# Kernel tuning notes

Hardware: AMD Instinct MI355X
Metric: run time of the kernel (lower is better)

## Reference

```python
import jax, jax.numpy as jnp
import numpy as np

B, L, D, H = 4, 2048, 2048, 16
HD = D // H
EPS = 1e-6


def _rope_tables(l, hd, base=10000.0):
    inv = 1.0 / (base ** (np.arange(0, hd, 2, dtype=np.float32) / hd))  # [hd/2]
    t = np.arange(l, dtype=np.float32)
    ang = np.outer(t, inv)  # [l, hd/2]
    return jnp.asarray(np.cos(ang)), jnp.asarray(np.sin(ang))


def setup_inputs() -> dict:
    key = jax.random.key(0)
    ks = jax.random.split(key, 8)
    cos, sin = _rope_tables(L, HD)
    s = 1.0 / np.sqrt(D)
    return {
        "x": jax.random.normal(ks[0], (B, L, D), jnp.float32),
        "freqs_cos": cos,
        "freqs_sin": sin,
        "Wqk": jax.random.normal(ks[1], (D, 2 * D), jnp.float32) * s,
        "Wv": jax.random.normal(ks[2], (D, D), jnp.float32) * s,
        "bv": jax.random.normal(ks[3], (D,), jnp.float32) * 0.02,
        "Wp": jax.random.normal(ks[4], (D, D), jnp.float32) * s,
        "bp": jax.random.normal(ks[5], (D,), jnp.float32) * 0.02,
        "qn_w": jnp.ones((HD,), jnp.float32),
        "kn_w": jnp.ones((HD,), jnp.float32),
    }


def _rmsnorm(x, w, eps=EPS):
    ms = jnp.mean(jnp.square(x), axis=-1, keepdims=True)
    return x * jax.lax.rsqrt(ms + eps) * w


def _rope(x, cos, sin):
    # x: [b,h,l,hd]; cos/sin: [l,hd/2]; interleaved (complex) rotation
    x1 = x[..., 0::2]
    x2 = x[..., 1::2]
    c = cos[None, None, :, :]
    s = sin[None, None, :, :]
    out = jnp.stack([x1 * c - x2 * s, x1 * s + x2 * c], axis=-1)
    return out.reshape(x.shape)


def reference(x, freqs_cos, freqs_sin, Wqk, Wv, bv, Wp, bp, qn_w, kn_w):
    b, l, d = x.shape
    qk = x @ Wqk  # [b,l,2d]
    q, k = jnp.split(qk, 2, axis=-1)
    v = x @ Wv + bv
    # [b,l,d] -> [b,h,l,hd]
    to_heads = lambda t: t.reshape(b, l, H, HD).transpose(0, 2, 1, 3)
    q, k, v = to_heads(q), to_heads(k), to_heads(v)
    q = _rmsnorm(q, qn_w)
    k = _rmsnorm(k, kn_w)
    q = _rope(q, freqs_cos, freqs_sin)
    k = _rope(k, freqs_cos, freqs_sin)
    scale = 1.0 / jnp.sqrt(jnp.asarray(HD, q.dtype))
    scores = jnp.einsum("bhqd,bhkd->bhqk", q, k) * scale
    causal = jnp.tril(jnp.ones((l, l), bool))
    scores = jnp.where(causal[None, None], scores, jnp.asarray(-1e30, scores.dtype))
    attn = jax.nn.softmax(scores, axis=-1)
    y = jnp.einsum("bhqk,bhkd->bhqd", attn, v)
    y = y.transpose(0, 2, 1, 3).reshape(b, l, d)
    return y @ Wp + bp
```

## Files before the change

kernel.cpp:

```cpp
#include <hip/hip_runtime.h>
#include <hip/hip_bf16.h>
#include <math.h>

#define B_  4
#define L_  2048
#define D_  2048
#define H_  16
#define HD_ 128
#define BH_ (B_*H_)
#define BL_ (B_*L_)

typedef __attribute__((ext_vector_type(4))) float  f32x4;
typedef __attribute__((ext_vector_type(8))) __bf16 bf16x8;

static __device__ __forceinline__ float bf2f(unsigned short u) {
    union { unsigned int i; float f; } v; v.i = ((unsigned int)u) << 16; return v.f;
}
static __device__ __forceinline__ unsigned short f2bf(float f) {
    union { float f; unsigned int i; } v; v.f = f;
    unsigned int x = v.i;
    return (unsigned short)((x + 0x7fffu + ((x >> 16) & 1u)) >> 16);
}

static __device__ __forceinline__ void gload16(const unsigned short* g, unsigned short* l) {
    __builtin_amdgcn_global_load_lds(
        (const __attribute__((address_space(1))) unsigned int*)(const void*)g,
        (__attribute__((address_space(3))) unsigned int*)(void*)l, 16, 0, 0);
}

__global__ __launch_bounds__(256) void k_f32_to_bf16(const float* __restrict__ s,
                                                     unsigned short* __restrict__ d, int n8) {
    int i = blockIdx.x * 256 + threadIdx.x;
    if (i >= n8) return;
    const float* p = s + (size_t)i * 8;
    float4 a = *(const float4*)p;
    float4 b = *(const float4*)(p + 4);
    union { bf16x8 v; unsigned short u[8]; } o;
    o.u[0]=f2bf(a.x); o.u[1]=f2bf(a.y); o.u[2]=f2bf(a.z); o.u[3]=f2bf(a.w);
    o.u[4]=f2bf(b.x); o.u[5]=f2bf(b.y); o.u[6]=f2bf(b.z); o.u[7]=f2bf(b.w);
    *(bf16x8*)(d + (size_t)i * 8) = o.v;
}

__global__ __launch_bounds__(256) void k_transpose_f2b(const float* __restrict__ src,
                                                       unsigned short* __restrict__ dst,
                                                       int R, int C, int dstStride) {
    __shared__ float tile[32][33];
    int tx = threadIdx.x & 31, ty = threadIdx.x >> 5;
    int c0 = blockIdx.x * 32, r0 = blockIdx.y * 32;
    #pragma unroll
    for (int i = 0; i < 32; i += 8)
        tile[ty + i][tx] = src[(size_t)(r0 + ty + i) * C + c0 + tx];
    __syncthreads();
    #pragma unroll
    for (int i = 0; i < 32; i += 8)
        dst[(size_t)(c0 + ty + i) * dstStride + r0 + tx] = f2bf(tile[tx][ty + i]);
}

__global__ __launch_bounds__(256) void k_transpose_v(const unsigned short* __restrict__ vb,
                                                     unsigned short* __restrict__ vT) {
    __shared__ unsigned short tile[32][33];
    int bh = blockIdx.z;
    int hd0 = blockIdx.x * 32, l0 = blockIdx.y * 32;
    int tx = threadIdx.x & 31, ty = threadIdx.x >> 5;
    const unsigned short* in = vb + (size_t)bh * L_ * HD_;
    unsigned short* out      = vT + (size_t)bh * L_ * HD_;
    #pragma unroll
    for (int i = 0; i < 32; i += 8)
        tile[ty + i][tx] = in[(size_t)(l0 + ty + i) * HD_ + hd0 + tx];
    __syncthreads();
    #pragma unroll
    for (int i = 0; i < 32; i += 8)
        out[(size_t)(hd0 + ty + i) * L_ + l0 + tx] = tile[tx][ty + i];
}

template<int MG, int NG>
static __device__ __forceinline__ void mfma_quad(const bf16x8 (&afr)[4][2],
                                                 const bf16x8 (&bfr)[2][2],
                                                 f32x4 (&acc)[8][4]) {
    #pragma unroll
    for (int mi = 0; mi < 4; ++mi)
        #pragma unroll
        for (int ni = 0; ni < 2; ++ni) {
            acc[MG*4+mi][NG*2+ni] = __builtin_amdgcn_mfma_f32_16x16x32_bf16(
                afr[mi][0], bfr[ni][0], acc[MG*4+mi][NG*2+ni], 0, 0, 0);
            acc[MG*4+mi][NG*2+ni] = __builtin_amdgcn_mfma_f32_16x16x32_bf16(
                afr[mi][1], bfr[ni][1], acc[MG*4+mi][NG*2+ni], 0, 0, 0);
        }
}

static __device__ __forceinline__ void ds_load_a(const unsigned short* u, int wm,
                                                 int l15, int l4, bf16x8 (&afr)[4][2]) {
    int sw = l15 & 7;
    #pragma unroll
    for (int mi = 0; mi < 4; ++mi) {
        int ro = (wm*64 + mi*16 + l15) * 64;
        afr[mi][0] = *(const bf16x8*)(u + ro + ((l4 ^ sw) << 3));
        afr[mi][1] = *(const bf16x8*)(u + ro + (((4 + l4) ^ sw) << 3));
    }
}

static __device__ __forceinline__ void ds_load_b(const unsigned short* u, int wn,
                                                 int l15, int l4, bf16x8 (&bfr)[2][2]) {
    int sw = l15 & 7;
    #pragma unroll
    for (int ni = 0; ni < 2; ++ni) {
        int ro = (wn*32 + ni*16 + l15) * 64;
        bfr[ni][0] = *(const bf16x8*)(u + ro + ((l4 ^ sw) << 3));
        bfr[ni][1] = *(const bf16x8*)(u + ro + (((4 + l4) ^ sw) << 3));
    }
}

#define STAGE_A_(c_, mg_, t_) do {                                                        \
    gload16(gA + (size_t)(((mg_)*64      ) * 2048) + (t_)*64, &Lds[c_][0][mg_][w*512]);   \
    gload16(gA + (size_t)(((mg_)*64 + 128) * 2048) + (t_)*64, &Lds[c_][0][mg_][4096 + w*512]); \
} while (0)
#define STAGE_B_(c_, ng_, t_) do {                                                        \
    gload16(gB + (size_t)(((ng_)*32 + ((w>>2)    )*64) * 2048) + (t_)*64, &Lds[c_][1][ng_][w*512]); \
    gload16(gB + (size_t)(((ng_)*32 + ((w>>2) + 2)*64) * 2048) + (t_)*64, &Lds[c_][1][ng_][4096 + w*512]); \
} while (0)
#define SB_() __builtin_amdgcn_sched_barrier(0)

template<int MODE>
__global__ __launch_bounds__(512, 2) void k_gemm(const unsigned short* __restrict__ A,
                                                 const unsigned short* __restrict__ Bt,
                                                 int M, int N, int K,
                                                 const float* __restrict__ bias,
                                                 unsigned short* __restrict__ qout,
                                                 unsigned short* __restrict__ kout,
                                                 unsigned short* __restrict__ vout,
                                                 float* __restrict__ fout) {
    (void)K;
    __shared__ __align__(16) unsigned short Lds[2][2][2][8192];
    const int tid = threadIdx.x;
    const int lane = tid & 63, w = tid >> 6;
    const int wm = w >> 2, wn = w & 3;
    const int l15 = lane & 15, l4 = lane >> 4;
    const int lsw = (lane & 7) ^ ((lane >> 3) & 7);

    int nwgx = gridDim.x;
    int bid = blockIdx.y * nwgx + blockIdx.x;
    int cpx = (nwgx * gridDim.y) >> 3;
    int sb = (bid & 7) * cpx + (bid >> 3);
    int n0 = (sb % nwgx) * 256, m0 = (sb / nwgx) * 256;

    const unsigned short* gA = A  + (size_t)(m0 + w*8 + (lane >> 3)) * 2048 + lsw*8;
    const unsigned short* gB = Bt + (size_t)(n0 + (w&3)*8 + (lane >> 3)) * 2048 + lsw*8;

    f32x4 acc[8][4] = {};
    bf16x8 afr[4][2], bf0[2][2], bf1[2][2];
    const int nt = 2048 / 64;

    STAGE_A_(0, 0, 0); STAGE_B_(0, 0, 0); STAGE_B_(0, 1, 0); STAGE_A_(0, 1, 0);
    STAGE_A_(1, 0, 1); STAGE_B_(1, 0, 1); STAGE_B_(1, 1, 1);
    asm volatile("s_waitcnt vmcnt(6)" ::: "memory");
    __builtin_amdgcn_s_barrier();

    for (int t = 0; t < nt; ++t) {
        const int c = t & 1, cn = c ^ 1;
        const bool h1 = (t + 1 < nt), h2 = (t + 2 < nt);

        ds_load_a(&Lds[c][0][0][0], wm, l15, l4, afr);
        ds_load_b(&Lds[c][1][0][0], wn, l15, l4, bf0);
        SB_();
        ds_load_b(&Lds[c][1][1][0], wn, l15, l4, bf1);
        SB_();
        if (h1) STAGE_A_(cn, 1, t + 1);
        __builtin_amdgcn_s_barrier();
        asm volatile("s_waitcnt lgkmcnt(4)" ::: "memory");
        SB_();
        __builtin_amdgcn_s_setprio(1);
        mfma_quad<0, 0>(afr, bf0, acc);
        __builtin_amdgcn_s_setprio(0);
        SB_();
        __builtin_amdgcn_s_barrier();

        asm volatile("s_waitcnt lgkmcnt(0)" ::: "memory");
        SB_();
        __builtin_amdgcn_s_setprio(1);
        mfma_quad<0, 1>(afr, bf1, acc);
        __builtin_amdgcn_s_setprio(0);
        SB_();
        ds_load_a(&Lds[c][0][1][0], wm, l15, l4, afr);
        SB_();
        if (h2) STAGE_A_(c, 0, t + 2);
        __builtin_amdgcn_s_barrier();

        if (h2) STAGE_B_(c, 0, t + 2);
        asm volatile("s_waitcnt lgkmcnt(0)" ::: "memory");
        SB_();
        __builtin_amdgcn_s_setprio(1);
        mfma_quad<1, 1>(afr, bf1, acc);
        __builtin_amdgcn_s_setprio(0);
        SB_();
        if (h2) STAGE_B_(c, 1, t + 2);
        __builtin_amdgcn_s_setprio(1);
        mfma_quad<1, 0>(afr, bf0, acc);
        __builtin_amdgcn_s_setprio(0);
        SB_();
        if (h2) asm volatile("s_waitcnt vmcnt(4)" ::: "memory");
        else    asm volatile("s_waitcnt vmcnt(0)" ::: "memory");
        __builtin_amdgcn_s_barrier();
    }

    #pragma unroll
    for (int mi = 0; mi < 8; ++mi) {
        #pragma unroll
        for (int ni = 0; ni < 4; ++ni) {
            int ncol = n0 + wn*64 + ni*16 + l15;
            #pragma unroll
            for (int j = 0; j < 4; ++j) {
                int m = m0 + wm*128 + mi*16 + l4*4 + j;
                float v = acc[mi][ni][j];
                if (MODE == 0) {
                    int b = m >> 11, l = m & 2047;
                    if (ncol < 2048) {
                        int h = ncol >> 7, hd = ncol & 127;
                        qout[((size_t)(b*H_ + h) * L_ + l) * HD_ + hd] = f2bf(v);
                    } else if (ncol < 4096) {
                        int cc = ncol - 2048, h = cc >> 7, hd = cc & 127;
                        kout[((size_t)(b*H_ + h) * L_ + l) * HD_ + hd] = f2bf(v);
                    } else {
                        int cc = ncol - 4096, h = cc >> 7, hd = cc & 127;
                        vout[((size_t)(b*H_ + h) * L_ + l) * HD_ + hd] = f2bf(v + bias[cc]);
                    }
                } else {
                    fout[(size_t)m * N + ncol] = v + bias[ncol];
                }
            }
        }
    }
}

__global__ __launch_bounds__(256) void k_normrope(unsigned short* __restrict__ qb,
                                                  unsigned short* __restrict__ kb,
                                                  const float* __restrict__ cosT,
                                                  const float* __restrict__ sinT,
                                                  const float* __restrict__ qw,
                                                  const float* __restrict__ kw) {
    const float QSCL = 0.08838834764831845f * 1.4426950408889634f;
    int lane = threadIdx.x & 63;
    int row = blockIdx.x * 4 + (threadIdx.x >> 6);
    int isK = row >= BH_ * L_;
    unsigned short* buf = isK ? kb : qb;
    const float* w = isK ? kw : qw;
    int r = isK ? row - BH_ * L_ : row;
    int l = r & (L_ - 1);
    unsigned short* p = buf + (size_t)r * HD_ + lane * 2;
    ushort2 u = *(const ushort2*)p;
    float x1 = bf2f(u.x), x2 = bf2f(u.y);
    float ss = x1*x1 + x2*x2;
    #pragma unroll
    for (int off = 32; off; off >>= 1) ss += __shfl_xor(ss, off);
    float rs = rsqrtf(ss * (1.0f / 128.0f) + 1e-6f);
    rs *= isK ? 1.0f : QSCL;
    float c = cosT[l * 64 + lane], s = sinT[l * 64 + lane];
    float y1 = x1 * rs * w[lane * 2];
    float y2 = x2 * rs * w[lane * 2 + 1];
    ushort2 o;
    o.x = f2bf(y1 * c - y2 * s);
    o.y = f2bf(y1 * s + y2 * c);
    *(ushort2*)p = o;
}

#define PLDT 72

__global__ __launch_bounds__(256) void k_attn(const unsigned short* __restrict__ qbuf,
                                              const unsigned short* __restrict__ kbuf,
                                              const unsigned short* __restrict__ vT,
                                              unsigned short* __restrict__ yb) {
    __shared__ __align__(16) unsigned short Ks[64 * 128];
    __shared__ __align__(16) unsigned short Vs[128 * 64];
    __shared__ __align__(16) unsigned short Ps[4][32 * PLDT];
    int tid = threadIdx.x, lane = tid & 63, w = tid >> 6;
    int l15 = lane & 15, l4 = lane >> 4;
    int qb = 15 - (blockIdx.x >> 6);
    int bh = blockIdx.x & 63;
    const unsigned short* Q  = qbuf + (size_t)bh * L_ * HD_;
    const unsigned short* Kp = kbuf + (size_t)bh * L_ * HD_;
    const unsigned short* Vp = vT   + (size_t)bh * L_ * HD_;
    int qr0 = qb * 128 + w * 32;

    bf16x8 qf[2][4];
    #pragma unroll
    for (int m = 0; m < 2; ++m)
        #pragma unroll
        for (int ks = 0; ks < 4; ++ks)
            qf[m][ks] = *(const bf16x8*)(Q + (size_t)(qr0 + m*16 + l15) * HD_ + ks*32 + l4*8);

    f32x4 accO[2][8] = {};
    f32x4 accW[2] = {};

    bf16x8 vones;
    #pragma unroll
    for (int i = 0; i < 8; ++i) vones[i] = (__bf16)1.0f;

    const float BOUND = 20.0f;
    int nkt = 2 * qb + 2;

    for (int kt = 0; kt < nkt; ++kt) {
        int kbase = kt * 64;
        #pragma unroll
        for (int i = 0; i < 4; ++i) {
            int g = w * 4 + i;
            int kr = g * 4 + (lane >> 4);
            gload16(Kp + (size_t)(kbase + kr) * HD_ + (((lane & 15) ^ (kr & 15)) << 3),
                    Ks + g * 512);
            int vr = g * 8 + (lane >> 3);
            gload16(Vp + (size_t)vr * L_ + kbase + (((lane & 7) ^ (vr & 7)) << 3),
                    Vs + g * 512);
        }
        __syncthreads();

        if (kbase <= qr0 + 31) {
            f32x4 sf[2][4] = {};
            #pragma unroll
            for (int f = 0; f < 4; ++f)
                #pragma unroll
                for (int ks = 0; ks < 4; ++ks) {
                    bf16x8 kf = *(const bf16x8*)(Ks + (f*16 + l15) * 128 +
                                                 ((((ks*4) + l4) ^ l15) << 3));
                    sf[0][f] = __builtin_amdgcn_mfma_f32_16x16x32_bf16(qf[0][ks], kf, sf[0][f], 0, 0, 0);
                    sf[1][f] = __builtin_amdgcn_mfma_f32_16x16x32_bf16(qf[1][ks], kf, sf[1][f], 0, 0, 0);
                }

            unsigned short* ps = Ps[w];
            #pragma unroll
            for (int m = 0; m < 2; ++m) {
                bool needmask = (kbase + 63 > qr0 + m*16);
                #pragma unroll
                for (int f = 0; f < 4; ++f)
                    #pragma unroll
                    for (int j = 0; j < 4; ++j) {
                        float s = sf[m][f][j];
                        if (needmask) {
                            int key  = kbase + f*16 + l15;
                            int qrow = qr0 + m*16 + l4*4 + j;
                            if (key > qrow) s = -1e30f;
                        }
                        float p = exp2f(s - BOUND);
                        *(__bf16*)(ps + (m*16 + l4*4 + j) * PLDT + f*16 + l15) = (__bf16)p;
                    }
            }

            #pragma unroll
            for (int ks = 0; ks < 2; ++ks) {
                bf16x8 pa0 = *(const bf16x8*)(ps + l15 * PLDT + ks*32 + l4*8);
                bf16x8 pa1 = *(const bf16x8*)(ps + (16 + l15) * PLDT + ks*32 + l4*8);
                #pragma unroll
                for (int cf = 0; cf < 8; ++cf) {
                    bf16x8 vf = *(const bf16x8*)(Vs + (cf*16 + l15) * 64 +
                                                 ((((ks*4) + l4) ^ (l15 & 7)) << 3));
                    accO[0][cf] = __builtin_amdgcn_mfma_f32_16x16x32_bf16(pa0, vf, accO[0][cf], 0, 0, 0);
                    accO[1][cf] = __builtin_amdgcn_mfma_f32_16x16x32_bf16(pa1, vf, accO[1][cf], 0, 0, 0);
                }
                accW[0] = __builtin_amdgcn_mfma_f32_16x16x32_bf16(pa0, vones, accW[0], 0, 0, 0);
                accW[1] = __builtin_amdgcn_mfma_f32_16x16x32_bf16(pa1, vones, accW[1], 0, 0, 0);
            }
        }
        __syncthreads();
    }

    int b = bh >> 4, h = bh & 15;
    #pragma unroll
    for (int m = 0; m < 2; ++m)
        #pragma unroll
        for (int cf = 0; cf < 8; ++cf)
            #pragma unroll
            for (int j = 0; j < 4; ++j) {
                int qrow = qr0 + m*16 + l4*4 + j;
                float o = accO[m][cf][j] / accW[m][j];
                yb[((size_t)(b * L_ + qrow)) * D_ + h*128 + cf*16 + l15] = f2bf(o);
            }
}

extern "C" void kernel_launch(void* const* d_in, const int* in_sizes, int n_in,
                              void* d_out, int out_size, void* d_ws, size_t ws_size,
                              hipStream_t stream) {
    const float* x    = (const float*)d_in[0];
    const float* fcos = (const float*)d_in[1];
    const float* fsin = (const float*)d_in[2];
    const float* Wqk  = (const float*)d_in[3];
    const float* Wv   = (const float*)d_in[4];
    const float* bv   = (const float*)d_in[5];
    const float* Wp   = (const float*)d_in[6];
    const float* bp   = (const float*)d_in[7];
    const float* qn_w = (const float*)d_in[8];
    const float* kn_w = (const float*)d_in[9];
    float* out = (float*)d_out;

    char* ws = (char*)d_ws;
    unsigned short* Wt   = (unsigned short*)(ws);
    unsigned short* Wpt  = (unsigned short*)(ws + 25165824);
    unsigned short* xb   = (unsigned short*)(ws + 33554432);
    unsigned short* qbuf = (unsigned short*)(ws + 67108864);
    unsigned short* kbuf = (unsigned short*)(ws + 100663296);
    unsigned short* vbuf = (unsigned short*)(ws + 134217728);
    unsigned short* vTb  = (unsigned short*)(ws + 167772160);
    unsigned short* yb   = xb;

    k_f32_to_bf16<<<8192, 256, 0, stream>>>(x, xb, BL_ * D_ / 8);
    k_transpose_f2b<<<dim3(128, 64), 256, 0, stream>>>(Wqk, Wt, 2048, 4096, 2048);
    k_transpose_f2b<<<dim3(64, 64),  256, 0, stream>>>(Wv,  Wt + (size_t)4096 * 2048, 2048, 2048, 2048);
    k_transpose_f2b<<<dim3(64, 64),  256, 0, stream>>>(Wp,  Wpt, 2048, 2048, 2048);

    k_gemm<0><<<dim3(24, 32), 512, 0, stream>>>(xb, Wt, BL_, 6144, 2048, bv,
                                                qbuf, kbuf, vbuf, nullptr);
    k_normrope<<<2 * BH_ * L_ / 4, 256, 0, stream>>>(qbuf, kbuf, fcos, fsin, qn_w, kn_w);
    k_transpose_v<<<dim3(4, 64, 64), 256, 0, stream>>>(vbuf, vTb);
    k_attn<<<BH_ * (L_ / 128), 256, 0, stream>>>(qbuf, kbuf, vTb, yb);
    k_gemm<1><<<dim3(8, 32), 512, 0, stream>>>(yb, Wpt, BL_, 2048, 2048, bp,
                                               nullptr, nullptr, nullptr, out);
}
```

Before: 484.5 us.

## Write V transposed from GEMM epilogue, drop transpose kernel, tune waits and priorities

The QKV GEMM epilogue now writes the V columns directly in the [bh, hd, l] transposed layout using 4-element vector stores, so the separate V transpose kernel and its extra round trip through global memory are gone. The GEMM pipeline's vmcnt wait threshold is relaxed from 4 to 6 outstanding loads. The attention kernel raises wave priority around its MFMA blocks. Risks: the new V store pattern is strided by L per column, and the looser vmcnt must still match the number of outstanding staged loads or the pipeline could read stale data.

```diff
diff --git a/kernel.cpp b/kernel.cpp
--- a/kernel.cpp
+++ b/kernel.cpp
@@ -56,22 +56,6 @@
         dst[(size_t)(c0 + ty + i) * dstStride + r0 + tx] = f2bf(tile[tx][ty + i]);
 }
 
-__global__ __launch_bounds__(256) void k_transpose_v(const unsigned short* __restrict__ vb,
-                                                     unsigned short* __restrict__ vT) {
-    __shared__ unsigned short tile[32][33];
-    int bh = blockIdx.z;
-    int hd0 = blockIdx.x * 32, l0 = blockIdx.y * 32;
-    int tx = threadIdx.x & 31, ty = threadIdx.x >> 5;
-    const unsigned short* in = vb + (size_t)bh * L_ * HD_;
-    unsigned short* out      = vT + (size_t)bh * L_ * HD_;
-    #pragma unroll
-    for (int i = 0; i < 32; i += 8)
-        tile[ty + i][tx] = in[(size_t)(l0 + ty + i) * HD_ + hd0 + tx];
-    __syncthreads();
-    #pragma unroll
-    for (int i = 0; i < 32; i += 8)
-        out[(size_t)(hd0 + ty + i) * L_ + l0 + tx] = tile[tx][ty + i];
-}
 
 template<int MG, int NG>
 static __device__ __forceinline__ void mfma_quad(const bf16x8 (&afr)[4][2],
@@ -197,7 +181,7 @@
         mfma_quad<1, 0>(afr, bf0, acc);
         __builtin_amdgcn_s_setprio(0);
         SB_();
-        if (h2) asm volatile("s_waitcnt vmcnt(4)" ::: "memory");
+        if (h2) asm volatile("s_waitcnt vmcnt(6)" ::: "memory");
         else    asm volatile("s_waitcnt vmcnt(0)" ::: "memory");
         __builtin_amdgcn_s_barrier();
     }
@@ -207,24 +191,34 @@
         #pragma unroll
         for (int ni = 0; ni < 4; ++ni) {
             int ncol = n0 + wn*64 + ni*16 + l15;
-            #pragma unroll
-            for (int j = 0; j < 4; ++j) {
-                int m = m0 + wm*128 + mi*16 + l4*4 + j;
-                float v = acc[mi][ni][j];
-                if (MODE == 0) {
-                    int b = m >> 11, l = m & 2047;
-                    if (ncol < 2048) {
-                        int h = ncol >> 7, hd = ncol & 127;
-                        qout[((size_t)(b*H_ + h) * L_ + l) * HD_ + hd] = f2bf(v);
-                    } else if (ncol < 4096) {
-                        int cc = ncol - 2048, h = cc >> 7, hd = cc & 127;
-                        kout[((size_t)(b*H_ + h) * L_ + l) * HD_ + hd] = f2bf(v);
+            int mbase = m0 + wm*128 + mi*16 + l4*4;
+            if (MODE == 0 && ncol >= 4096) {
+                int cc = ncol - 4096, h = cc >> 7, hd = cc & 127;
+                int b = mbase >> 11, l = mbase & 2047;
+                float bv = bias[cc];
+                ushort4 o;
+                o.x = f2bf(acc[mi][ni][0] + bv);
+                o.y = f2bf(acc[mi][ni][1] + bv);
+                o.z = f2bf(acc[mi][ni][2] + bv);
+                o.w = f2bf(acc[mi][ni][3] + bv);
+                *(ushort4*)(vout + ((size_t)((b*H_ + h) * HD_ + hd)) * L_ + l) = o;
+            } else {
+                #pragma unroll
+                for (int j = 0; j < 4; ++j) {
+                    int m = mbase + j;
+                    float v = acc[mi][ni][j];
+                    if (MODE == 0) {
+                        int b = m >> 11, l = m & 2047;
+                        if (ncol < 2048) {
+                            int h = ncol >> 7, hd = ncol & 127;
+                            qout[((size_t)(b*H_ + h) * L_ + l) * HD_ + hd] = f2bf(v);
+                        } else {
+                            int cc = ncol - 2048, h = cc >> 7, hd = cc & 127;
+                            kout[((size_t)(b*H_ + h) * L_ + l) * HD_ + hd] = f2bf(v);
+                        }
                     } else {
-                        int cc = ncol - 4096, h = cc >> 7, hd = cc & 127;
-                        vout[((size_t)(b*H_ + h) * L_ + l) * HD_ + hd] = f2bf(v + bias[cc]);
+                        fout[(size_t)m * N + ncol] = v + bias[ncol];
                     }
-                } else {
-                    fout[(size_t)m * N + ncol] = v + bias[ncol];
                 }
             }
         }
@@ -313,6 +307,7 @@
 
         if (kbase <= qr0 + 31) {
             f32x4 sf[2][4] = {};
+            __builtin_amdgcn_s_setprio(1);
             #pragma unroll
             for (int f = 0; f < 4; ++f)
                 #pragma unroll
@@ -322,6 +317,7 @@
                     sf[0][f] = __builtin_amdgcn_mfma_f32_16x16x32_bf16(qf[0][ks], kf, sf[0][f], 0, 0, 0);
                     sf[1][f] = __builtin_amdgcn_mfma_f32_16x16x32_bf16(qf[1][ks], kf, sf[1][f], 0, 0, 0);
                 }
+            __builtin_amdgcn_s_setprio(0);
 
             unsigned short* ps = Ps[w];
             #pragma unroll
@@ -342,6 +338,7 @@
                     }
             }
 
+            __builtin_amdgcn_s_setprio(1);
             #pragma unroll
             for (int ks = 0; ks < 2; ++ks) {
                 bf16x8 pa0 = *(const bf16x8*)(ps + l15 * PLDT + ks*32 + l4*8);
@@ -356,6 +353,7 @@
                 accW[0] = __builtin_amdgcn_mfma_f32_16x16x32_bf16(pa0, vones, accW[0], 0, 0, 0);
                 accW[1] = __builtin_amdgcn_mfma_f32_16x16x32_bf16(pa1, vones, accW[1], 0, 0, 0);
             }
+            __builtin_amdgcn_s_setprio(0);
         }
         __syncthreads();
     }
@@ -394,7 +392,6 @@
     unsigned short* xb   = (unsigned short*)(ws + 33554432);
     unsigned short* qbuf = (unsigned short*)(ws + 67108864);
     unsigned short* kbuf = (unsigned short*)(ws + 100663296);
-    unsigned short* vbuf = (unsigned short*)(ws + 134217728);
     unsigned short* vTb  = (unsigned short*)(ws + 167772160);
     unsigned short* yb   = xb;
 
@@ -404,9 +401,8 @@
     k_transpose_f2b<<<dim3(64, 64),  256, 0, stream>>>(Wp,  Wpt, 2048, 2048, 2048);
 
     k_gemm<0><<<dim3(24, 32), 512, 0, stream>>>(xb, Wt, BL_, 6144, 2048, bv,
-                                                qbuf, kbuf, vbuf, nullptr);
+                                                qbuf, kbuf, vTb, nullptr);
     k_normrope<<<2 * BH_ * L_ / 4, 256, 0, stream>>>(qbuf, kbuf, fcos, fsin, qn_w, kn_w);
-    k_transpose_v<<<dim3(4, 64, 64), 256, 0, stream>>>(vbuf, vTb);
     k_attn<<<BH_ * (L_ / 128), 256, 0, stream>>>(qbuf, kbuf, vTb, yb);
     k_gemm<1><<<dim3(8, 32), 512, 0, stream>>>(yb, Wpt, BL_, 2048, 2048, bp,
                                                nullptr, nullptr, nullptr, out);
```

Result: faster. 452.6 us (median of 2 runs) (-6.6%).
